# Kernel optimization log

Measured on AMD Instinct MI355X. Metric: run time of the kernel, lower is better.

Reference implementation:

```python
import jax, jax.numpy as jnp
import numpy as np

MIN_ROUGHNESS = 0.08
MAX_ROUGHNESS = 0.5
N_MIPS = 6  # 512 -> 16 cubemap mip chain


def _safe_normalize(x, eps=1e-20):
    return x * jax.lax.rsqrt(jnp.clip(jnp.sum(x * x, -1, keepdims=True), eps, None))


def _dot(a, b):
    return jnp.sum(a * b, -1, keepdims=True)


def _cube_face_uv(d):
    # nvdiffrast cube addressing (matches util.cube_to_dir face layout)
    x, y, z = d[..., 0], d[..., 1], d[..., 2]
    ax, ay, az = jnp.abs(x), jnp.abs(y), jnp.abs(z)
    is_x = (ax >= ay) & (ax >= az)
    is_y = (~is_x) & (ay >= az)
    face = jnp.where(is_x, jnp.where(x >= 0, 0, 1),
           jnp.where(is_y, jnp.where(y >= 0, 2, 3), jnp.where(z >= 0, 4, 5)))
    ma = jnp.maximum(jnp.where(is_x, ax, jnp.where(is_y, ay, az)), 1e-20)
    u = jnp.where(face == 0, -z, jnp.where(face == 1, z, jnp.where(face == 5, -x, x))) / ma
    v = jnp.where(face == 2, z, jnp.where(face == 3, -z, -y)) / ma
    return face, u, v


def _bilinear_cube(tex, face, u, v):
    # tex: [6,R,R,C]; face/u/v: [...]; edge-clamped bilinear within the face
    R = tex.shape[1]
    tu = (u * 0.5 + 0.5) * R - 0.5
    tv = (v * 0.5 + 0.5) * R - 0.5
    x0 = jnp.floor(tu); y0 = jnp.floor(tv)
    fx = (tu - x0)[..., None]; fy = (tv - y0)[..., None]
    x0i = jnp.clip(x0, 0, R - 1).astype(jnp.int32)
    x1i = jnp.clip(x0 + 1, 0, R - 1).astype(jnp.int32)
    y0i = jnp.clip(y0, 0, R - 1).astype(jnp.int32)
    y1i = jnp.clip(y0 + 1, 0, R - 1).astype(jnp.int32)
    c00 = tex[face, y0i, x0i]; c01 = tex[face, y0i, x1i]
    c10 = tex[face, y1i, x0i]; c11 = tex[face, y1i, x1i]
    return (c00 * (1 - fx) + c01 * fx) * (1 - fy) + (c10 * (1 - fx) + c11 * fx) * fy


def _sample_cubemap(tex, dirs):
    f, u, v = _cube_face_uv(dirs)
    return _bilinear_cube(tex, f, u, v)


def _sample_2d_clamp(tex, uv):
    # tex: [H,W,C]; uv in [0,1]^2, clamp boundary bilinear (FG LUT lookup)
    H, W = tex.shape[0], tex.shape[1]
    tu = uv[..., 0] * W - 0.5
    tv = uv[..., 1] * H - 0.5
    x0 = jnp.floor(tu); y0 = jnp.floor(tv)
    fx = (tu - x0)[..., None]; fy = (tv - y0)[..., None]
    x0i = jnp.clip(x0, 0, W - 1).astype(jnp.int32)
    x1i = jnp.clip(x0 + 1, 0, W - 1).astype(jnp.int32)
    y0i = jnp.clip(y0, 0, H - 1).astype(jnp.int32)
    y1i = jnp.clip(y0 + 1, 0, H - 1).astype(jnp.int32)
    c00 = tex[y0i, x0i]; c01 = tex[y0i, x1i]
    c10 = tex[y1i, x0i]; c11 = tex[y1i, x1i]
    return (c00 * (1 - fx) + c01 * fx) * (1 - fy) + (c10 * (1 - fx) + c11 * fx) * fy


def _get_mip(r, n_levels):
    lo = (jnp.clip(r, MIN_ROUGHNESS, MAX_ROUGHNESS) - MIN_ROUGHNESS) / (MAX_ROUGHNESS - MIN_ROUGHNESS) * (n_levels - 2)
    hi = (jnp.clip(r, MAX_ROUGHNESS, 1.0) - MAX_ROUGHNESS) / (1.0 - MAX_ROUGHNESS) + (n_levels - 2)
    return jnp.where(r < MAX_ROUGHNESS, lo, hi)


def _linear2srgb(x):
    xs = jnp.where(x > 0.0031308, x, 1.0)  # avoid pow(0) grad issues
    return jnp.where(x > 0.0031308, 1.055 * jnp.power(xs, 1.0 / 2.4) - 0.055, 12.92 * x)


def _avg_pool_cube(c):
    F, R, _, C = c.shape
    return c.reshape(F, R // 2, 2, R // 2, 2, C).mean(axis=(2, 4))


def setup_inputs() -> dict:
    key = jax.random.key(0)
    ks = jax.random.split(key, 10)
    B, H, W = 1, 1024, 1024
    gb_pos = jax.random.normal(ks[0], (B, H, W, 3), jnp.float32)
    gb_normal = _safe_normalize(jax.random.normal(ks[1], (B, H, W, 3), jnp.float32))
    basecolor = jax.random.uniform(ks[2], (B, H, W, 3), jnp.float32)
    metallic = jax.random.uniform(ks[3], (B, H, W, 1), jnp.float32)
    roughness = jax.random.uniform(ks[4], (B, H, W, 1), jnp.float32)
    view_pos = jax.random.normal(ks[5], (1, 1, 1, 3), jnp.float32) * 3.0
    diffuse = jax.random.uniform(ks[6], (6, 16, 16, 3), jnp.float32)
    fg_lut = jax.random.uniform(ks[7], (256, 256, 2), jnp.float32)
    specs = {}
    s = jax.random.uniform(ks[8], (6, 512, 512, 3), jnp.float32)
    for l in range(N_MIPS):
        specs['spec%d' % l] = s
        if l < N_MIPS - 1:
            s = _avg_pool_cube(s)
    return dict(gb_pos=gb_pos, gb_normal=gb_normal, basecolor=basecolor,
                metallic=metallic, roughness=roughness, view_pos=view_pos,
                diffuse=diffuse, fg_lut=fg_lut, **specs)


def reference(gb_pos, gb_normal, basecolor, metallic, roughness, view_pos,
              diffuse, fg_lut, spec0, spec1, spec2, spec3, spec4, spec5):
    specs = [spec0, spec1, spec2, spec3, spec4, spec5]
    L = len(specs)
    metallic = metallic[..., :1]
    wo = _safe_normalize(view_pos - gb_pos)
    diffuse_albedo = (1.0 - metallic) * basecolor
    specular_albedo = 0.04 * (1.0 - metallic) + metallic * basecolor
    reflvec = _safe_normalize(2.0 * _dot(wo, gb_normal) * gb_normal - wo)
    # diffuse IBL: cubemap gather along normal
    ambient = _sample_cubemap(diffuse, gb_normal)
    diffuse_linear = ambient * diffuse_albedo
    # FG LUT gather
    NdotV = jnp.clip(_dot(wo, gb_normal), 1e-4, None)
    fg = _sample_2d_clamp(fg_lut, jnp.concatenate([NdotV, roughness], -1))
    # trilinear (linear-mipmap-linear) specular cubemap gather
    mip = jnp.clip(_get_mip(roughness[..., 0], L), 0.0, L - 1.0)
    face, u, v = _cube_face_uv(reflvec)
    spec = jnp.zeros(gb_pos.shape[:-1] + (spec0.shape[-1],), gb_pos.dtype)
    for l in range(L):
        w = jnp.clip(1.0 - jnp.abs(mip - l), 0.0, 1.0)[..., None]
        spec = spec + w * _bilinear_cube(specs[l], face, u, v)
    reflectance = specular_albedo * fg[..., 0:1] + fg[..., 1:2]
    rgb = spec * reflectance + diffuse_linear
    return _linear2srgb(jnp.clip(rgb, 0.0, 1.0))
```

## Files before the change

### kernel.cpp

```cpp
#include <hip/hip_runtime.h>
#include <hip/hip_fp16.h>

struct V3 { float x, y, z; };

__device__ __forceinline__ V3 v3add(V3 a, V3 b){ return {a.x+b.x, a.y+b.y, a.z+b.z}; }
__device__ __forceinline__ V3 v3sub(V3 a, V3 b){ return {a.x-b.x, a.y-b.y, a.z-b.z}; }
__device__ __forceinline__ V3 v3scale(V3 a, float s){ return {a.x*s, a.y*s, a.z*s}; }
__device__ __forceinline__ V3 v3mul(V3 a, V3 b){ return {a.x*b.x, a.y*b.y, a.z*b.z}; }
__device__ __forceinline__ float dot3(V3 a, V3 b){ return fmaf(a.x,b.x, fmaf(a.y,b.y, a.z*b.z)); }
__device__ __forceinline__ V3 nrm3(V3 a){
    float s = rsqrtf(fmaxf(dot3(a,a), 1e-20f));
    return v3scale(a, s);
}

struct __align__(16) PairBlock { __half2 h01, h23, h45, h67; };

#define OFF0 0
#define OFF1 1572864
#define OFF2 1966080
#define OFF3 2064384
#define OFF4 2088960
#define OFF5 2095104
#define DIFF_OFF 2096640
#define FG_OFF 2098176
#define TOTAL_BLOCKS 2163712
#define PACK_ONLY_BLOCKS 2098176
#define WS_BYTES_FULL  ((size_t)TOTAL_BLOCKS * 16)
#define WS_BYTES_PACK  ((size_t)PACK_ONLY_BLOCKS * 16)

__device__ __forceinline__ void cube_face_uv(V3 d, int& face, float& u, float& v){
    float ax = fabsf(d.x), ay = fabsf(d.y), az = fabsf(d.z);
    bool is_x = (ax >= ay) && (ax >= az);
    bool is_y = (!is_x) && (ay >= az);
    face = is_x ? (d.x >= 0.f ? 0 : 1)
                : (is_y ? (d.y >= 0.f ? 2 : 3)
                        : (d.z >= 0.f ? 4 : 5));
    float ma = fmaxf(is_x ? ax : (is_y ? ay : az), 1e-20f);
    float un = (face == 0) ? -d.z : (face == 1) ? d.z : (face == 5) ? -d.x : d.x;
    float vn = (face == 2) ?  d.z : (face == 3) ? -d.z : -d.y;
    float inv = 1.0f / ma;
    u = un * inv;
    v = vn * inv;
}

__device__ __forceinline__ void pair_extract(const PairBlock& pb, V3& lo, V3& hi){
    lo.x = __low2float(pb.h01);  lo.y = __high2float(pb.h01); lo.z = __low2float(pb.h23);
    hi.x = __high2float(pb.h23); hi.y = __low2float(pb.h45);  hi.z = __high2float(pb.h45);
}

__device__ __forceinline__ V3 bilinear_pairtex(const PairBlock* __restrict__ lvl, int R,
                                               int face, float u, float v){
    float Rf = (float)R;
    float tu = fmaf(fmaf(u, 0.5f, 0.5f), Rf, -0.5f);
    float tv = fmaf(fmaf(v, 0.5f, 0.5f), Rf, -0.5f);
    float x0f = floorf(tu), y0f = floorf(tv);
    float fx = tu - x0f,    fy = tv - y0f;
    int x0 = (int)x0f;
    fx = (x0 < 0) ? 0.f : fx;
    int xb  = min(max(x0, 0), R-1);
    int y0i = min(max((int)y0f,     0), R-1);
    int y1i = min(max((int)y0f + 1, 0), R-1);
    const PairBlock* fb = lvl + (size_t)face * R * R;
    PairBlock b0 = fb[(size_t)y0i * R + xb];
    PairBlock b1 = fb[(size_t)y1i * R + xb];
    V3 l0, h0, l1, h1;
    pair_extract(b0, l0, h0);
    pair_extract(b1, l1, h1);
    V3 r0 = { l0.x + (h0.x-l0.x)*fx, l0.y + (h0.y-l0.y)*fx, l0.z + (h0.z-l0.z)*fx };
    V3 r1 = { l1.x + (h1.x-l1.x)*fx, l1.y + (h1.y-l1.y)*fx, l1.z + (h1.z-l1.z)*fx };
    return { r0.x + (r1.x-r0.x)*fy, r0.y + (r1.y-r0.y)*fy, r0.z + (r1.z-r0.z)*fy };
}

__device__ __forceinline__ void sample_fg_pair(const float4* __restrict__ fgp,
                                               float u, float v, float& fa, float& fb){
    const int W = 256, H = 256;
    float tu = fmaf(u, (float)W, -0.5f);
    float tv = fmaf(v, (float)H, -0.5f);
    float x0f = floorf(tu), y0f = floorf(tv);
    float fx = tu - x0f,    fy = tv - y0f;
    int x0 = (int)x0f;
    fx = (x0 < 0) ? 0.f : fx;
    int xb  = min(max(x0, 0), W-1);
    int y0i = min(max((int)y0f,     0), H-1);
    int y1i = min(max((int)y0f + 1, 0), H-1);
    float4 r0 = fgp[(size_t)y0i * W + xb];
    float4 r1 = fgp[(size_t)y1i * W + xb];
    float t0a = r0.x + (r0.z - r0.x)*fx, t0b = r0.y + (r0.w - r0.y)*fx;
    float t1a = r1.x + (r1.z - r1.x)*fx, t1b = r1.y + (r1.w - r1.y)*fx;
    fa = t0a + (t1a - t0a)*fy;
    fb = t0b + (t1b - t0b)*fy;
}

__device__ __forceinline__ void sample_fg(const float* __restrict__ lut,
                                          float u, float v, float& fa, float& fb){
    const int W = 256, H = 256;
    float tu = fmaf(u, (float)W, -0.5f);
    float tv = fmaf(v, (float)H, -0.5f);
    float x0 = floorf(tu), y0 = floorf(tv);
    float fx = tu - x0,    fy = tv - y0;
    int x0i = min(max((int)x0,     0), W-1);
    int x1i = min(max((int)x0 + 1, 0), W-1);
    int y0i = min(max((int)y0,     0), H-1);
    int y1i = min(max((int)y0 + 1, 0), H-1);
    const float2* l2 = (const float2*)lut;
    float2 a = l2[(size_t)y0i*W + x0i];
    float2 b = l2[(size_t)y0i*W + x1i];
    float2 d = l2[(size_t)y1i*W + x0i];
    float2 e = l2[(size_t)y1i*W + x1i];
    float w00 = (1.f-fx)*(1.f-fy), w01 = fx*(1.f-fy);
    float w10 = (1.f-fx)*fy,       w11 = fx*fy;
    fa = a.x*w00 + b.x*w01 + d.x*w10 + e.x*w11;
    fb = a.y*w00 + b.y*w01 + d.y*w10 + e.y*w11;
}

__device__ __forceinline__ V3 bilinear_cube3(const float* __restrict__ tex, int R,
                                             int face, float u, float v){
    float Rf = (float)R;
    float tu = fmaf(fmaf(u, 0.5f, 0.5f), Rf, -0.5f);
    float tv = fmaf(fmaf(v, 0.5f, 0.5f), Rf, -0.5f);
    float x0 = floorf(tu), y0 = floorf(tv);
    float fx = tu - x0,    fy = tv - y0;
    int x0i = min(max((int)x0,     0), R-1);
    int x1i = min(max((int)x0 + 1, 0), R-1);
    int y0i = min(max((int)y0,     0), R-1);
    int y1i = min(max((int)y0 + 1, 0), R-1);
    const float* base = tex + (size_t)face * R * R * 3;
    const float* r0 = base + (size_t)y0i * R * 3;
    const float* r1 = base + (size_t)y1i * R * 3;
    float a0 = r0[3*x0i], a1 = r0[3*x0i+1], a2 = r0[3*x0i+2];
    float b0 = r0[3*x1i], b1 = r0[3*x1i+1], b2 = r0[3*x1i+2];
    float d0 = r1[3*x0i], d1 = r1[3*x0i+1], d2 = r1[3*x0i+2];
    float e0 = r1[3*x1i], e1 = r1[3*x1i+1], e2 = r1[3*x1i+2];
    float w00 = (1.f-fx)*(1.f-fy), w01 = fx*(1.f-fy);
    float w10 = (1.f-fx)*fy,       w11 = fx*fy;
    V3 out;
    out.x = a0*w00 + b0*w01 + d0*w10 + e0*w11;
    out.y = a1*w00 + b1*w01 + d1*w10 + e1*w11;
    out.z = a2*w00 + b2*w01 + d2*w10 + e2*w11;
    return out;
}

__device__ __forceinline__ float lin2srgb(float x){
    float xs = (x > 0.0031308f) ? x : 1.0f;
    float p  = __builtin_amdgcn_exp2f(__builtin_amdgcn_logf(xs) * (1.0f/2.4f));
    return (x > 0.0031308f) ? fmaf(1.055f, p, -0.055f) : 12.92f * x;
}

__device__ __forceinline__ float clamp01(float x){ return fminf(fmaxf(x, 0.f), 1.f); }

__global__ __launch_bounds__(256)
void pack_kernel(const float* __restrict__ s0, const float* __restrict__ s1,
                 const float* __restrict__ s2, const float* __restrict__ s3,
                 const float* __restrict__ s4, const float* __restrict__ s5,
                 const float* __restrict__ diffuse, const float* __restrict__ fg_lut,
                 PairBlock* __restrict__ ws, int total)
{
    int t = blockIdx.x * blockDim.x + threadIdx.x;
    if (t >= total) return;
    if (t >= FG_OFF) {
        int local = t - FG_OFF;
        int x = local & 255;
        int nb = (x == 255) ? local : local + 1;
        float4 v = make_float4(fg_lut[2*local], fg_lut[2*local+1],
                               fg_lut[2*nb],    fg_lut[2*nb+1]);
        ((float4*)ws)[t] = v;
        return;
    }
    const float* src; int local; int Rmask;
    if      (t >= DIFF_OFF) { src = diffuse; local = t - DIFF_OFF; Rmask = 15;  }
    else if (t >= OFF5)     { src = s5;      local = t - OFF5;     Rmask = 15;  }
    else if (t >= OFF4)     { src = s4;      local = t - OFF4;     Rmask = 31;  }
    else if (t >= OFF3)     { src = s3;      local = t - OFF3;     Rmask = 63;  }
    else if (t >= OFF2)     { src = s2;      local = t - OFF2;     Rmask = 127; }
    else if (t >= OFF1)     { src = s1;      local = t - OFF1;     Rmask = 255; }
    else                    { src = s0;      local = t;            Rmask = 511; }
    int nb = ((local & Rmask) == Rmask) ? local : local + 1;
    float ar = src[3*local], ag = src[3*local+1], ab = src[3*local+2];
    float br = src[3*nb],    bg = src[3*nb+1],    bb = src[3*nb+2];
    PairBlock pb;
    pb.h01 = __floats2half2_rn(ar, ag);
    pb.h23 = __floats2half2_rn(ab, br);
    pb.h45 = __floats2half2_rn(bg, bb);
    pb.h67 = __floats2half2_rn(0.f, 0.f);
    ws[t] = pb;
}

struct PixPre {
    V3 diff_alb, spec_alb;
    int sface; float su, sv;
    int dface; float du, dv;
    int offA, RA, offB, RB; float f;
    float ndotv, rough;
};

__device__ __forceinline__ PixPre pre_pixel(
    int i,
    const float* __restrict__ gb_pos, const float* __restrict__ gb_normal,
    const float* __restrict__ basecolor, const float* __restrict__ metallic,
    const float* __restrict__ roughness, V3 vp)
{
    V3 pos = { gb_pos[3*i],    gb_pos[3*i+1],    gb_pos[3*i+2] };
    V3 nrm = { gb_normal[3*i], gb_normal[3*i+1], gb_normal[3*i+2] };
    V3 bc  = { basecolor[3*i], basecolor[3*i+1], basecolor[3*i+2] };
    float m = metallic[i];
    float r = roughness[i];

    V3 wo = nrm3(v3sub(vp, pos));
    float ndv_raw = dot3(wo, nrm);
    V3 refl = nrm3(v3sub(v3scale(nrm, 2.0f*ndv_raw), wo));

    PixPre p;
    float one_m = 1.0f - m;
    p.diff_alb = v3scale(bc, one_m);
    p.spec_alb = { fmaf(m, bc.x, 0.04f*one_m),
                   fmaf(m, bc.y, 0.04f*one_m),
                   fmaf(m, bc.z, 0.04f*one_m) };
    p.ndotv = fmaxf(ndv_raw, 0.0001f);
    p.rough = r;

    const float MIN_R = 0.08f, MAX_R = 0.5f;
    float lo = (fminf(fmaxf(r, MIN_R), MAX_R) - MIN_R) / (MAX_R - MIN_R) * 4.0f;
    float hi = (fminf(fmaxf(r, MAX_R), 1.0f) - MAX_R) / (1.0f - MAX_R) + 4.0f;
    float mip = (r < MAX_R) ? lo : hi;
    mip = fminf(fmaxf(mip, 0.0f), 5.0f);
    int l0 = min((int)mip, 5);
    p.f = mip - (float)l0;
    int l1 = min(l0 + 1, 5);

    int offA = OFF0;
    offA = (l0 == 1) ? OFF1 : offA; offA = (l0 == 2) ? OFF2 : offA;
    offA = (l0 == 3) ? OFF3 : offA; offA = (l0 == 4) ? OFF4 : offA;
    offA = (l0 == 5) ? OFF5 : offA;
    int offB = OFF0;
    offB = (l1 == 1) ? OFF1 : offB; offB = (l1 == 2) ? OFF2 : offB;
    offB = (l1 == 3) ? OFF3 : offB; offB = (l1 == 4) ? OFF4 : offB;
    offB = (l1 == 5) ? OFF5 : offB;
    p.offA = offA; p.RA = 512 >> l0;
    p.offB = offB; p.RB = 512 >> l1;

    cube_face_uv(nrm, p.dface, p.du, p.dv);
    cube_face_uv(refl, p.sface, p.su, p.sv);
    return p;
}

template <bool FGPAIR>
__device__ __forceinline__ void finish_pixel(
    int i, const PixPre& p,
    const PairBlock* __restrict__ ws, const PairBlock* __restrict__ lds_diff,
    const float* __restrict__ fg_lut, float* __restrict__ out)
{
    V3 specA = bilinear_pairtex(ws + p.offA, p.RA, p.sface, p.su, p.sv);
    V3 specB = bilinear_pairtex(ws + p.offB, p.RB, p.sface, p.su, p.sv);
    V3 ambient = bilinear_pairtex(lds_diff, 16, p.dface, p.du, p.dv);
    float fa, fb;
    if (FGPAIR) sample_fg_pair((const float4*)(ws + FG_OFF), p.ndotv, p.rough, fa, fb);
    else        sample_fg(fg_lut, p.ndotv, p.rough, fa, fb);

    V3 spec = { specA.x + (specB.x - specA.x) * p.f,
                specA.y + (specB.y - specA.y) * p.f,
                specA.z + (specB.z - specA.z) * p.f };
    V3 reflc = { fmaf(p.spec_alb.x, fa, fb),
                 fmaf(p.spec_alb.y, fa, fb),
                 fmaf(p.spec_alb.z, fa, fb) };
    V3 rgb = v3add(v3mul(spec, reflc), v3mul(ambient, p.diff_alb));

    out[3*i+0] = lin2srgb(clamp01(rgb.x));
    out[3*i+1] = lin2srgb(clamp01(rgb.y));
    out[3*i+2] = lin2srgb(clamp01(rgb.z));
}

template <bool FGPAIR>
__global__ __launch_bounds__(256)
void envlight_packed(const float* __restrict__ gb_pos,
                     const float* __restrict__ gb_normal,
                     const float* __restrict__ basecolor,
                     const float* __restrict__ metallic,
                     const float* __restrict__ roughness,
                     const float* __restrict__ view_pos,
                     const float* __restrict__ fg_lut,
                     const PairBlock* __restrict__ ws,
                     float* __restrict__ out,
                     int n, int half)
{
    __shared__ PairBlock lds_diff[1536];
    for (int t = threadIdx.x; t < 1536; t += 256)
        lds_diff[t] = ws[DIFF_OFF + t];
    __syncthreads();

    int i = blockIdx.x * blockDim.x + threadIdx.x;
    if (i >= half) return;
    int j = i + half;

    V3 vp = { view_pos[0], view_pos[1], view_pos[2] };

    PixPre pa = pre_pixel(i, gb_pos, gb_normal, basecolor, metallic, roughness, vp);
    if (j < n) {
        PixPre pb = pre_pixel(j, gb_pos, gb_normal, basecolor, metallic, roughness, vp);
        finish_pixel<FGPAIR>(i, pa, ws, lds_diff, fg_lut, out);
        finish_pixel<FGPAIR>(j, pb, ws, lds_diff, fg_lut, out);
    } else {
        finish_pixel<FGPAIR>(i, pa, ws, lds_diff, fg_lut, out);
    }
}

__global__ __launch_bounds__(256)
void envlight_fallback(const float* __restrict__ gb_pos,
                       const float* __restrict__ gb_normal,
                       const float* __restrict__ basecolor,
                       const float* __restrict__ metallic,
                       const float* __restrict__ roughness,
                       const float* __restrict__ view_pos,
                       const float* __restrict__ diffuse,
                       const float* __restrict__ fg_lut,
                       const float* __restrict__ s0, const float* __restrict__ s1,
                       const float* __restrict__ s2, const float* __restrict__ s3,
                       const float* __restrict__ s4, const float* __restrict__ s5,
                       float* __restrict__ out, int n)
{
    int i = blockIdx.x * blockDim.x + threadIdx.x;
    if (i >= n) return;
    V3 vp = { view_pos[0], view_pos[1], view_pos[2] };
    PixPre p = pre_pixel(i, gb_pos, gb_normal, basecolor, metallic, roughness, vp);
    int l0 = 0;
    l0 = (p.offA == OFF1) ? 1 : l0; l0 = (p.offA == OFF2) ? 2 : l0;
    l0 = (p.offA == OFF3) ? 3 : l0; l0 = (p.offA == OFF4) ? 4 : l0;
    l0 = (p.offA == OFF5) ? 5 : l0;
    int l1 = 0;
    l1 = (p.offB == OFF1) ? 1 : l1; l1 = (p.offB == OFF2) ? 2 : l1;
    l1 = (p.offB == OFF3) ? 3 : l1; l1 = (p.offB == OFF4) ? 4 : l1;
    l1 = (p.offB == OFF5) ? 5 : l1;
    const float* tA = s0;
    tA = (l0 == 1) ? s1 : tA; tA = (l0 == 2) ? s2 : tA;
    tA = (l0 == 3) ? s3 : tA; tA = (l0 == 4) ? s4 : tA; tA = (l0 == 5) ? s5 : tA;
    const float* tB = s0;
    tB = (l1 == 1) ? s1 : tB; tB = (l1 == 2) ? s2 : tB;
    tB = (l1 == 3) ? s3 : tB; tB = (l1 == 4) ? s4 : tB; tB = (l1 == 5) ? s5 : tB;
    V3 ambient = bilinear_cube3(diffuse, 16, p.dface, p.du, p.dv);
    V3 specA   = bilinear_cube3(tA, p.RA, p.sface, p.su, p.sv);
    V3 specB   = bilinear_cube3(tB, p.RB, p.sface, p.su, p.sv);
    float fa, fb;
    sample_fg(fg_lut, p.ndotv, p.rough, fa, fb);
    V3 spec = { specA.x + (specB.x - specA.x) * p.f,
                specA.y + (specB.y - specA.y) * p.f,
                specA.z + (specB.z - specA.z) * p.f };
    V3 reflc = { fmaf(p.spec_alb.x, fa, fb),
                 fmaf(p.spec_alb.y, fa, fb),
                 fmaf(p.spec_alb.z, fa, fb) };
    V3 rgb = v3add(v3mul(spec, reflc), v3mul(ambient, p.diff_alb));
    out[3*i+0] = lin2srgb(clamp01(rgb.x));
    out[3*i+1] = lin2srgb(clamp01(rgb.y));
    out[3*i+2] = lin2srgb(clamp01(rgb.z));
}

extern "C" void kernel_launch(void* const* d_in, const int* in_sizes, int n_in,
                              void* d_out, int out_size, void* d_ws, size_t ws_size,
                              hipStream_t stream) {
    const float* gb_pos    = (const float*)d_in[0];
    const float* gb_normal = (const float*)d_in[1];
    const float* basecolor = (const float*)d_in[2];
    const float* metallic  = (const float*)d_in[3];
    const float* roughness = (const float*)d_in[4];
    const float* view_pos  = (const float*)d_in[5];
    const float* diffuse   = (const float*)d_in[6];
    const float* fg_lut    = (const float*)d_in[7];
    const float* s0        = (const float*)d_in[8];
    const float* s1        = (const float*)d_in[9];
    const float* s2        = (const float*)d_in[10];
    const float* s3        = (const float*)d_in[11];
    const float* s4        = (const float*)d_in[12];
    const float* s5        = (const float*)d_in[13];
    float* out = (float*)d_out;

    int n = in_sizes[0] / 3;
    int block = 256;

    bool full = ws_size >= WS_BYTES_FULL;
    bool mid  = ws_size >= WS_BYTES_PACK;
    if (full || mid) {
        PairBlock* ws = (PairBlock*)d_ws;
        int total = full ? TOTAL_BLOCKS : PACK_ONLY_BLOCKS;
        int pgrid = (total + block - 1) / block;
        pack_kernel<<<pgrid, block, 0, stream>>>(s0, s1, s2, s3, s4, s5,
                                                 diffuse, fg_lut, ws, total);
        int half = (n + 1) / 2;
        int grid = (half + block - 1) / block;
        if (full)
            envlight_packed<true><<<grid, block, 0, stream>>>(gb_pos, gb_normal,
                basecolor, metallic, roughness, view_pos, fg_lut, ws, out, n, half);
        else
            envlight_packed<false><<<grid, block, 0, stream>>>(gb_pos, gb_normal,
                basecolor, metallic, roughness, view_pos, fg_lut, ws, out, n, half);
    } else {
        int grid = (n + block - 1) / block;
        envlight_fallback<<<grid, block, 0, stream>>>(gb_pos, gb_normal, basecolor,
            metallic, roughness, view_pos, diffuse, fg_lut,
            s0, s1, s2, s3, s4, s5, out, n);
    }
}
```

Measured before the change: 167.6 us.

## Pack full 2x2 bilinear quads per texel so each sample is one 32-byte fetch

Adds a new packing kernel that stores, for every texel of every specular mip, the diffuse cubemap and the FG LUT, the full 2x2 bilinear footprint in fp16 (32 bytes per texel, 16 for FG). The main kernel then fetches each bilinear sample with two adjacent float4 loads instead of two row loads. It also drops the two-pixels-per-thread scheme and the LDS staging of the diffuse map in favour of one pixel per thread. The cost is a workspace twice as large and a heavier pack pass writing about 67 MB, plus fp16 rounding of the FG LUT, all in exchange for fewer scattered gathers in the shading kernel.

```diff
diff --git a/kernel.cpp b/kernel.cpp
--- a/kernel.cpp
+++ b/kernel.cpp
@@ -13,7 +13,8 @@
     return v3scale(a, s);
 }
 
-struct __align__(16) PairBlock { __half2 h01, h23, h45, h67; };
+__device__ __forceinline__ __half2 as_h2(float f){ union { float f; __half2 h; } u; u.f = f; return u.h; }
+__device__ __forceinline__ float   as_f(__half2 h){ union { float f; __half2 h; } u; u.h = h; return u.f; }
 
 #define OFF0 0
 #define OFF1 1572864
@@ -22,11 +23,20 @@
 #define OFF4 2088960
 #define OFF5 2095104
 #define DIFF_OFF 2096640
+#define SPEC_DIFF_COUNT 2098176
+
+struct __align__(16) PairBlock { __half2 h01, h23, h45, h67; };
 #define FG_OFF 2098176
 #define TOTAL_BLOCKS 2163712
 #define PACK_ONLY_BLOCKS 2098176
 #define WS_BYTES_FULL  ((size_t)TOTAL_BLOCKS * 16)
 #define WS_BYTES_PACK  ((size_t)PACK_ONLY_BLOCKS * 16)
+
+#define QUAD_SPEC_BYTES ((size_t)SPEC_DIFF_COUNT * 32)
+#define QUAD_FG_COUNT   65536
+#define QUAD_FG_BYTES   ((size_t)QUAD_FG_COUNT * 16)
+#define WS_BYTES_QUAD   (QUAD_SPEC_BYTES + QUAD_FG_BYTES)
+#define QUAD_PACK_THREADS (SPEC_DIFF_COUNT + QUAD_FG_COUNT)
 
 __device__ __forceinline__ void cube_face_uv(V3 d, int& face, float& u, float& v){
     float ax = fabsf(d.x), ay = fabsf(d.y), az = fabsf(d.z);
@@ -41,6 +51,45 @@
     float inv = 1.0f / ma;
     u = un * inv;
     v = vn * inv;
+}
+
+__device__ __forceinline__ void quad_coord_cube(float u, float v, int R,
+                                                int& xq, int& yq, float& fx, float& fy){
+    float Rf = (float)R;
+    float tu = fmaf(fmaf(u, 0.5f, 0.5f), Rf, -0.5f);
+    float tv = fmaf(fmaf(v, 0.5f, 0.5f), Rf, -0.5f);
+    float x0f = floorf(tu), y0f = floorf(tv);
+    fx = tu - x0f; fy = tv - y0f;
+    int x0 = (int)x0f, y0 = (int)y0f;
+    fx = (x0 < 0) ? 0.f : fx;
+    fy = (y0 < 0) ? 0.f : fy;
+    xq = min(max(x0, 0), R-1);
+    yq = min(max(y0, 0), R-1);
+}
+
+__device__ __forceinline__ void quad_coord_2d(float u, float v, int W, int H,
+                                              int& xq, int& yq, float& fx, float& fy){
+    float tu = fmaf(u, (float)W, -0.5f);
+    float tv = fmaf(v, (float)H, -0.5f);
+    float x0f = floorf(tu), y0f = floorf(tv);
+    fx = tu - x0f; fy = tv - y0f;
+    int x0 = (int)x0f, y0 = (int)y0f;
+    fx = (x0 < 0) ? 0.f : fx;
+    fy = (y0 < 0) ? 0.f : fy;
+    xq = min(max(x0, 0), W-1);
+    yq = min(max(y0, 0), H-1);
+}
+
+__device__ __forceinline__ V3 quad_blend(float4 r0, float4 r1, float fx, float fy){
+    __half2 p0 = as_h2(r0.x), p1 = as_h2(r0.y), p2 = as_h2(r0.z);
+    __half2 q0 = as_h2(r1.x), q1 = as_h2(r1.y), q2 = as_h2(r1.z);
+    V3 t00 = { __low2float(p0),  __high2float(p0), __low2float(p1) };
+    V3 t01 = { __high2float(p1), __low2float(p2),  __high2float(p2) };
+    V3 t10 = { __low2float(q0),  __high2float(q0), __low2float(q1) };
+    V3 t11 = { __high2float(q1), __low2float(q2),  __high2float(q2) };
+    V3 r0v = { t00.x + (t01.x-t00.x)*fx, t00.y + (t01.y-t00.y)*fx, t00.z + (t01.z-t00.z)*fx };
+    V3 r1v = { t10.x + (t11.x-t10.x)*fx, t10.y + (t11.y-t10.y)*fx, t10.z + (t11.z-t10.z)*fx };
+    return { r0v.x + (r1v.x-r0v.x)*fy, r0v.y + (r1v.y-r0v.y)*fy, r0v.z + (r1v.z-r0v.z)*fy };
 }
 
 __device__ __forceinline__ void pair_extract(const PairBlock& pb, V3& lo, V3& hi){
@@ -89,28 +138,6 @@
     float t1a = r1.x + (r1.z - r1.x)*fx, t1b = r1.y + (r1.w - r1.y)*fx;
     fa = t0a + (t1a - t0a)*fy;
     fb = t0b + (t1b - t0b)*fy;
-}
-
-__device__ __forceinline__ void sample_fg(const float* __restrict__ lut,
-                                          float u, float v, float& fa, float& fb){
-    const int W = 256, H = 256;
-    float tu = fmaf(u, (float)W, -0.5f);
-    float tv = fmaf(v, (float)H, -0.5f);
-    float x0 = floorf(tu), y0 = floorf(tv);
-    float fx = tu - x0,    fy = tv - y0;
-    int x0i = min(max((int)x0,     0), W-1);
-    int x1i = min(max((int)x0 + 1, 0), W-1);
-    int y0i = min(max((int)y0,     0), H-1);
-    int y1i = min(max((int)y0 + 1, 0), H-1);
-    const float2* l2 = (const float2*)lut;
-    float2 a = l2[(size_t)y0i*W + x0i];
-    float2 b = l2[(size_t)y0i*W + x1i];
-    float2 d = l2[(size_t)y1i*W + x0i];
-    float2 e = l2[(size_t)y1i*W + x1i];
-    float w00 = (1.f-fx)*(1.f-fy), w01 = fx*(1.f-fy);
-    float w10 = (1.f-fx)*fy,       w11 = fx*fy;
-    fa = a.x*w00 + b.x*w01 + d.x*w10 + e.x*w11;
-    fb = a.y*w00 + b.y*w01 + d.y*w10 + e.y*w11;
 }
 
 __device__ __forceinline__ V3 bilinear_cube3(const float* __restrict__ tex, int R,
@@ -140,6 +167,28 @@
     return out;
 }
 
+__device__ __forceinline__ void sample_fg(const float* __restrict__ lut,
+                                          float u, float v, float& fa, float& fb){
+    const int W = 256, H = 256;
+    float tu = fmaf(u, (float)W, -0.5f);
+    float tv = fmaf(v, (float)H, -0.5f);
+    float x0 = floorf(tu), y0 = floorf(tv);
+    float fx = tu - x0,    fy = tv - y0;
+    int x0i = min(max((int)x0,     0), W-1);
+    int x1i = min(max((int)x0 + 1, 0), W-1);
+    int y0i = min(max((int)y0,     0), H-1);
+    int y1i = min(max((int)y0 + 1, 0), H-1);
+    const float2* l2 = (const float2*)lut;
+    float2 a = l2[(size_t)y0i*W + x0i];
+    float2 b = l2[(size_t)y0i*W + x1i];
+    float2 d = l2[(size_t)y1i*W + x0i];
+    float2 e = l2[(size_t)y1i*W + x1i];
+    float w00 = (1.f-fx)*(1.f-fy), w01 = fx*(1.f-fy);
+    float w10 = (1.f-fx)*fy,       w11 = fx*fy;
+    fa = a.x*w00 + b.x*w01 + d.x*w10 + e.x*w11;
+    fb = a.y*w00 + b.y*w01 + d.y*w10 + e.y*w11;
+}
+
 __device__ __forceinline__ float lin2srgb(float x){
     float xs = (x > 0.0031308f) ? x : 1.0f;
     float p  = __builtin_amdgcn_exp2f(__builtin_amdgcn_logf(xs) * (1.0f/2.4f));
@@ -147,6 +196,181 @@
 }
 
 __device__ __forceinline__ float clamp01(float x){ return fminf(fmaxf(x, 0.f), 1.f); }
+
+struct PixPre {
+    V3 diff_alb, spec_alb;
+    int sface; float su, sv;
+    int dface; float du, dv;
+    int offA, RA, offB, RB; float f;
+    float ndotv, rough;
+};
+
+__device__ __forceinline__ PixPre pre_pixel(
+    int i,
+    const float* __restrict__ gb_pos, const float* __restrict__ gb_normal,
+    const float* __restrict__ basecolor, const float* __restrict__ metallic,
+    const float* __restrict__ roughness, V3 vp)
+{
+    V3 pos = { gb_pos[3*i],    gb_pos[3*i+1],    gb_pos[3*i+2] };
+    V3 nrm = { gb_normal[3*i], gb_normal[3*i+1], gb_normal[3*i+2] };
+    V3 bc  = { basecolor[3*i], basecolor[3*i+1], basecolor[3*i+2] };
+    float m = metallic[i];
+    float r = roughness[i];
+
+    V3 wo = nrm3(v3sub(vp, pos));
+    float ndv_raw = dot3(wo, nrm);
+    V3 refl = nrm3(v3sub(v3scale(nrm, 2.0f*ndv_raw), wo));
+
+    PixPre p;
+    float one_m = 1.0f - m;
+    p.diff_alb = v3scale(bc, one_m);
+    p.spec_alb = { fmaf(m, bc.x, 0.04f*one_m),
+                   fmaf(m, bc.y, 0.04f*one_m),
+                   fmaf(m, bc.z, 0.04f*one_m) };
+    p.ndotv = fmaxf(ndv_raw, 0.0001f);
+    p.rough = r;
+
+    const float MIN_R = 0.08f, MAX_R = 0.5f;
+    float lo = (fminf(fmaxf(r, MIN_R), MAX_R) - MIN_R) / (MAX_R - MIN_R) * 4.0f;
+    float hi = (fminf(fmaxf(r, MAX_R), 1.0f) - MAX_R) / (1.0f - MAX_R) + 4.0f;
+    float mip = (r < MAX_R) ? lo : hi;
+    mip = fminf(fmaxf(mip, 0.0f), 5.0f);
+    int l0 = min((int)mip, 5);
+    p.f = mip - (float)l0;
+    int l1 = min(l0 + 1, 5);
+
+    int offA = OFF0;
+    offA = (l0 == 1) ? OFF1 : offA; offA = (l0 == 2) ? OFF2 : offA;
+    offA = (l0 == 3) ? OFF3 : offA; offA = (l0 == 4) ? OFF4 : offA;
+    offA = (l0 == 5) ? OFF5 : offA;
+    int offB = OFF0;
+    offB = (l1 == 1) ? OFF1 : offB; offB = (l1 == 2) ? OFF2 : offB;
+    offB = (l1 == 3) ? OFF3 : offB; offB = (l1 == 4) ? OFF4 : offB;
+    offB = (l1 == 5) ? OFF5 : offB;
+    p.offA = offA; p.RA = 512 >> l0;
+    p.offB = offB; p.RB = 512 >> l1;
+
+    cube_face_uv(nrm, p.dface, p.du, p.dv);
+    cube_face_uv(refl, p.sface, p.su, p.sv);
+    return p;
+}
+
+__global__ __launch_bounds__(256)
+void pack_quad_kernel(const float* __restrict__ s0, const float* __restrict__ s1,
+                      const float* __restrict__ s2, const float* __restrict__ s3,
+                      const float* __restrict__ s4, const float* __restrict__ s5,
+                      const float* __restrict__ diffuse, const float* __restrict__ fg_lut,
+                      float4* __restrict__ qtex ,
+                      float4* __restrict__ fgq  )
+{
+    int t = blockIdx.x * blockDim.x + threadIdx.x;
+    if (t >= QUAD_PACK_THREADS) return;
+    if (t >= SPEC_DIFF_COUNT) {
+        int local = t - SPEC_DIFF_COUNT;
+        int x = local & 255, y = local >> 8;
+        int i00 = local;
+        int i01 = (x == 255) ? local : local + 1;
+        int i10 = (y == 255) ? local : local + 256;
+        int i11 = (x == 255) ? i10 : i10 + 1;
+        float4 q = make_float4(
+            as_f(__floats2half2_rn(fg_lut[2*i00], fg_lut[2*i00+1])),
+            as_f(__floats2half2_rn(fg_lut[2*i01], fg_lut[2*i01+1])),
+            as_f(__floats2half2_rn(fg_lut[2*i10], fg_lut[2*i10+1])),
+            as_f(__floats2half2_rn(fg_lut[2*i11], fg_lut[2*i11+1])));
+        fgq[local] = q;
+        return;
+    }
+    const float* src; int local; int Rm, Rsh;
+    if      (t >= DIFF_OFF) { src = diffuse; local = t - DIFF_OFF; Rm = 15;  Rsh = 4; }
+    else if (t >= OFF5)     { src = s5;      local = t - OFF5;     Rm = 15;  Rsh = 4; }
+    else if (t >= OFF4)     { src = s4;      local = t - OFF4;     Rm = 31;  Rsh = 5; }
+    else if (t >= OFF3)     { src = s3;      local = t - OFF3;     Rm = 63;  Rsh = 6; }
+    else if (t >= OFF2)     { src = s2;      local = t - OFF2;     Rm = 127; Rsh = 7; }
+    else if (t >= OFF1)     { src = s1;      local = t - OFF1;     Rm = 255; Rsh = 8; }
+    else                    { src = s0;      local = t;            Rm = 511; Rsh = 9; }
+    int x = local & Rm;
+    int y = (local >> Rsh) & Rm;
+    int i00 = local;
+    int i01 = (x == Rm) ? local : local + 1;
+    int i10 = (y == Rm) ? local : local + (Rm + 1);
+    int i11 = (x == Rm) ? i10 : i10 + 1;
+    float a0 = src[3*i00], a1 = src[3*i00+1], a2 = src[3*i00+2];
+    float b0 = src[3*i01], b1 = src[3*i01+1], b2 = src[3*i01+2];
+    float c0 = src[3*i10], c1 = src[3*i10+1], c2 = src[3*i10+2];
+    float d0 = src[3*i11], d1 = src[3*i11+1], d2 = src[3*i11+2];
+    float4 row0 = make_float4(as_f(__floats2half2_rn(a0, a1)),
+                              as_f(__floats2half2_rn(a2, b0)),
+                              as_f(__floats2half2_rn(b1, b2)), 0.f);
+    float4 row1 = make_float4(as_f(__floats2half2_rn(c0, c1)),
+                              as_f(__floats2half2_rn(c2, d0)),
+                              as_f(__floats2half2_rn(d1, d2)), 0.f);
+    qtex[2*(size_t)t]     = row0;
+    qtex[2*(size_t)t + 1] = row1;
+}
+
+__global__ __launch_bounds__(256)
+void envlight_quad(const float* __restrict__ gb_pos,
+                   const float* __restrict__ gb_normal,
+                   const float* __restrict__ basecolor,
+                   const float* __restrict__ metallic,
+                   const float* __restrict__ roughness,
+                   const float* __restrict__ view_pos,
+                   const float4* __restrict__ qtex,
+                   const float4* __restrict__ fgq,
+                   float* __restrict__ out,
+                   int n)
+{
+    int i = blockIdx.x * blockDim.x + threadIdx.x;
+    if (i >= n) return;
+    V3 vp = { view_pos[0], view_pos[1], view_pos[2] };
+    PixPre p = pre_pixel(i, gb_pos, gb_normal, basecolor, metallic, roughness, vp);
+
+    int ax, ay; float afx, afy;
+    quad_coord_cube(p.su, p.sv, p.RA, ax, ay, afx, afy);
+    size_t qA = ((size_t)p.offA + (size_t)p.sface * p.RA * p.RA + (size_t)ay * p.RA + ax) * 2;
+
+    int bx, by; float bfx, bfy;
+    quad_coord_cube(p.su, p.sv, p.RB, bx, by, bfx, bfy);
+    size_t qB = ((size_t)p.offB + (size_t)p.sface * p.RB * p.RB + (size_t)by * p.RB + bx) * 2;
+
+    int dx, dy; float dfx, dfy;
+    quad_coord_cube(p.du, p.dv, 16, dx, dy, dfx, dfy);
+    size_t qD = ((size_t)DIFF_OFF + (size_t)p.dface * 256 + (size_t)dy * 16 + dx) * 2;
+
+    int fx_, fy_; float ffx, ffy;
+    quad_coord_2d(p.ndotv, p.rough, 256, 256, fx_, fy_, ffx, ffy);
+
+    float4 a0 = qtex[qA],   a1 = qtex[qA+1];
+    float4 b0 = qtex[qB],   b1 = qtex[qB+1];
+    float4 d0 = qtex[qD],   d1 = qtex[qD+1];
+    float4 fq = fgq[(size_t)fy_ * 256 + fx_];
+
+    V3 specA   = quad_blend(a0, a1, afx, afy);
+    V3 specB   = quad_blend(b0, b1, bfx, bfy);
+    V3 ambient = quad_blend(d0, d1, dfx, dfy);
+
+    __half2 f0 = as_h2(fq.x), f1 = as_h2(fq.y), f2 = as_h2(fq.z), f3 = as_h2(fq.w);
+    float t00a = __low2float(f0), t00b = __high2float(f0);
+    float t01a = __low2float(f1), t01b = __high2float(f1);
+    float t10a = __low2float(f2), t10b = __high2float(f2);
+    float t11a = __low2float(f3), t11b = __high2float(f3);
+    float r0a = t00a + (t01a - t00a)*ffx, r0b = t00b + (t01b - t00b)*ffx;
+    float r1a = t10a + (t11a - t10a)*ffx, r1b = t10b + (t11b - t10b)*ffx;
+    float fa = r0a + (r1a - r0a)*ffy;
+    float fb = r0b + (r1b - r0b)*ffy;
+
+    V3 spec = { specA.x + (specB.x - specA.x) * p.f,
+                specA.y + (specB.y - specA.y) * p.f,
+                specA.z + (specB.z - specA.z) * p.f };
+    V3 reflc = { fmaf(p.spec_alb.x, fa, fb),
+                 fmaf(p.spec_alb.y, fa, fb),
+                 fmaf(p.spec_alb.z, fa, fb) };
+    V3 rgb = v3add(v3mul(spec, reflc), v3mul(ambient, p.diff_alb));
+
+    out[3*i+0] = lin2srgb(clamp01(rgb.x));
+    out[3*i+1] = lin2srgb(clamp01(rgb.y));
+    out[3*i+2] = lin2srgb(clamp01(rgb.z));
+}
 
 __global__ __launch_bounds__(256)
 void pack_kernel(const float* __restrict__ s0, const float* __restrict__ s1,
@@ -185,77 +409,29 @@
     ws[t] = pb;
 }
 
-struct PixPre {
-    V3 diff_alb, spec_alb;
-    int sface; float su, sv;
-    int dface; float du, dv;
-    int offA, RA, offB, RB; float f;
-    float ndotv, rough;
-};
-
-__device__ __forceinline__ PixPre pre_pixel(
-    int i,
-    const float* __restrict__ gb_pos, const float* __restrict__ gb_normal,
-    const float* __restrict__ basecolor, const float* __restrict__ metallic,
-    const float* __restrict__ roughness, V3 vp)
+template <bool FGPAIR>
+__global__ __launch_bounds__(256)
+void envlight_pair(const float* __restrict__ gb_pos,
+                   const float* __restrict__ gb_normal,
+                   const float* __restrict__ basecolor,
+                   const float* __restrict__ metallic,
+                   const float* __restrict__ roughness,
+                   const float* __restrict__ view_pos,
+                   const float* __restrict__ fg_lut,
+                   const PairBlock* __restrict__ ws,
+                   float* __restrict__ out,
+                   int n)
 {
-    V3 pos = { gb_pos[3*i],    gb_pos[3*i+1],    gb_pos[3*i+2] };
-    V3 nrm = { gb_normal[3*i], gb_normal[3*i+1], gb_normal[3*i+2] };
-    V3 bc  = { basecolor[3*i], basecolor[3*i+1], basecolor[3*i+2] };
-    float m = metallic[i];
-    float r = roughness[i];
-
-    V3 wo = nrm3(v3sub(vp, pos));
-    float ndv_raw = dot3(wo, nrm);
-    V3 refl = nrm3(v3sub(v3scale(nrm, 2.0f*ndv_raw), wo));
-
-    PixPre p;
-    float one_m = 1.0f - m;
-    p.diff_alb = v3scale(bc, one_m);
-    p.spec_alb = { fmaf(m, bc.x, 0.04f*one_m),
-                   fmaf(m, bc.y, 0.04f*one_m),
-                   fmaf(m, bc.z, 0.04f*one_m) };
-    p.ndotv = fmaxf(ndv_raw, 0.0001f);
-    p.rough = r;
-
-    const float MIN_R = 0.08f, MAX_R = 0.5f;
-    float lo = (fminf(fmaxf(r, MIN_R), MAX_R) - MIN_R) / (MAX_R - MIN_R) * 4.0f;
-    float hi = (fminf(fmaxf(r, MAX_R), 1.0f) - MAX_R) / (1.0f - MAX_R) + 4.0f;
-    float mip = (r < MAX_R) ? lo : hi;
-    mip = fminf(fmaxf(mip, 0.0f), 5.0f);
-    int l0 = min((int)mip, 5);
-    p.f = mip - (float)l0;
-    int l1 = min(l0 + 1, 5);
-
-    int offA = OFF0;
-    offA = (l0 == 1) ? OFF1 : offA; offA = (l0 == 2) ? OFF2 : offA;
-    offA = (l0 == 3) ? OFF3 : offA; offA = (l0 == 4) ? OFF4 : offA;
-    offA = (l0 == 5) ? OFF5 : offA;
-    int offB = OFF0;
-    offB = (l1 == 1) ? OFF1 : offB; offB = (l1 == 2) ? OFF2 : offB;
-    offB = (l1 == 3) ? OFF3 : offB; offB = (l1 == 4) ? OFF4 : offB;
-    offB = (l1 == 5) ? OFF5 : offB;
-    p.offA = offA; p.RA = 512 >> l0;
-    p.offB = offB; p.RB = 512 >> l1;
-
-    cube_face_uv(nrm, p.dface, p.du, p.dv);
-    cube_face_uv(refl, p.sface, p.su, p.sv);
-    return p;
-}
-
-template <bool FGPAIR>
-__device__ __forceinline__ void finish_pixel(
-    int i, const PixPre& p,
-    const PairBlock* __restrict__ ws, const PairBlock* __restrict__ lds_diff,
-    const float* __restrict__ fg_lut, float* __restrict__ out)
-{
-    V3 specA = bilinear_pairtex(ws + p.offA, p.RA, p.sface, p.su, p.sv);
-    V3 specB = bilinear_pairtex(ws + p.offB, p.RB, p.sface, p.su, p.sv);
-    V3 ambient = bilinear_pairtex(lds_diff, 16, p.dface, p.du, p.dv);
+    int i = blockIdx.x * blockDim.x + threadIdx.x;
+    if (i >= n) return;
+    V3 vp = { view_pos[0], view_pos[1], view_pos[2] };
+    PixPre p = pre_pixel(i, gb_pos, gb_normal, basecolor, metallic, roughness, vp);
+    V3 specA   = bilinear_pairtex(ws + p.offA, p.RA, p.sface, p.su, p.sv);
+    V3 specB   = bilinear_pairtex(ws + p.offB, p.RB, p.sface, p.su, p.sv);
+    V3 ambient = bilinear_pairtex(ws + DIFF_OFF, 16, p.dface, p.du, p.dv);
     float fa, fb;
     if (FGPAIR) sample_fg_pair((const float4*)(ws + FG_OFF), p.ndotv, p.rough, fa, fb);
     else        sample_fg(fg_lut, p.ndotv, p.rough, fa, fb);
-
     V3 spec = { specA.x + (specB.x - specA.x) * p.f,
                 specA.y + (specB.y - specA.y) * p.f,
                 specA.z + (specB.z - specA.z) * p.f };
@@ -263,44 +439,9 @@
                  fmaf(p.spec_alb.y, fa, fb),
                  fmaf(p.spec_alb.z, fa, fb) };
     V3 rgb = v3add(v3mul(spec, reflc), v3mul(ambient, p.diff_alb));
-
     out[3*i+0] = lin2srgb(clamp01(rgb.x));
     out[3*i+1] = lin2srgb(clamp01(rgb.y));
     out[3*i+2] = lin2srgb(clamp01(rgb.z));
-}
-
-template <bool FGPAIR>
-__global__ __launch_bounds__(256)
-void envlight_packed(const float* __restrict__ gb_pos,
-                     const float* __restrict__ gb_normal,
-                     const float* __restrict__ basecolor,
-                     const float* __restrict__ metallic,
-                     const float* __restrict__ roughness,
-                     const float* __restrict__ view_pos,
-                     const float* __restrict__ fg_lut,
-                     const PairBlock* __restrict__ ws,
-                     float* __restrict__ out,
-                     int n, int half)
-{
-    __shared__ PairBlock lds_diff[1536];
-    for (int t = threadIdx.x; t < 1536; t += 256)
-        lds_diff[t] = ws[DIFF_OFF + t];
-    __syncthreads();
-
-    int i = blockIdx.x * blockDim.x + threadIdx.x;
-    if (i >= half) return;
-    int j = i + half;
-
-    V3 vp = { view_pos[0], view_pos[1], view_pos[2] };
-
-    PixPre pa = pre_pixel(i, gb_pos, gb_normal, basecolor, metallic, roughness, vp);
-    if (j < n) {
-        PixPre pb = pre_pixel(j, gb_pos, gb_normal, basecolor, metallic, roughness, vp);
-        finish_pixel<FGPAIR>(i, pa, ws, lds_diff, fg_lut, out);
-        finish_pixel<FGPAIR>(j, pb, ws, lds_diff, fg_lut, out);
-    } else {
-        finish_pixel<FGPAIR>(i, pa, ws, lds_diff, fg_lut, out);
-    }
 }
 
 __global__ __launch_bounds__(256)
@@ -373,25 +514,30 @@
 
     int n = in_sizes[0] / 3;
     int block = 256;
-
-    bool full = ws_size >= WS_BYTES_FULL;
-    bool mid  = ws_size >= WS_BYTES_PACK;
-    if (full || mid) {
+    int grid = (n + block - 1) / block;
+
+    if (ws_size >= WS_BYTES_QUAD) {
+        float4* qtex = (float4*)d_ws;
+        float4* fgq  = (float4*)((char*)d_ws + QUAD_SPEC_BYTES);
+        int pgrid = (QUAD_PACK_THREADS + block - 1) / block;
+        pack_quad_kernel<<<pgrid, block, 0, stream>>>(s0, s1, s2, s3, s4, s5,
+                                                      diffuse, fg_lut, qtex, fgq);
+        envlight_quad<<<grid, block, 0, stream>>>(gb_pos, gb_normal, basecolor,
+            metallic, roughness, view_pos, qtex, fgq, out, n);
+    } else if (ws_size >= WS_BYTES_PACK) {
+        bool full = ws_size >= WS_BYTES_FULL;
         PairBlock* ws = (PairBlock*)d_ws;
         int total = full ? TOTAL_BLOCKS : PACK_ONLY_BLOCKS;
         int pgrid = (total + block - 1) / block;
         pack_kernel<<<pgrid, block, 0, stream>>>(s0, s1, s2, s3, s4, s5,
                                                  diffuse, fg_lut, ws, total);
-        int half = (n + 1) / 2;
-        int grid = (half + block - 1) / block;
         if (full)
-            envlight_packed<true><<<grid, block, 0, stream>>>(gb_pos, gb_normal,
-                basecolor, metallic, roughness, view_pos, fg_lut, ws, out, n, half);
+            envlight_pair<true><<<grid, block, 0, stream>>>(gb_pos, gb_normal,
+                basecolor, metallic, roughness, view_pos, fg_lut, ws, out, n);
         else
-            envlight_packed<false><<<grid, block, 0, stream>>>(gb_pos, gb_normal,
-                basecolor, metallic, roughness, view_pos, fg_lut, ws, out, n, half);
+            envlight_pair<false><<<grid, block, 0, stream>>>(gb_pos, gb_normal,
+                basecolor, metallic, roughness, view_pos, fg_lut, ws, out, n);
     } else {
-        int grid = (n + block - 1) / block;
         envlight_fallback<<<grid, block, 0, stream>>>(gb_pos, gb_normal, basecolor,
             metallic, roughness, view_pos, diffuse, fg_lut,
             s0, s1, s2, s3, s4, s5, out, n);
```

Measured after the change: 168.6 us. Within noise of the previous version (+0.6%).
